# Optimization experiments

Measured on AMD Instinct MI355X. Metric: run time of the kernel, lower is better.

Reference implementation:

```python
import math
import jax, jax.numpy as jnp
import numpy as np

D_HEAD = 64
KS = 7
EPS = 1e-6


def _rope_freqs(d_head, n_heads):
    # AxialRoPE buffer: exp(linspace(log(pi), log(10*pi), nh*dim//4+1)[:-1]).view(dim//4, nh).T
    dim = d_head // 2
    n = n_heads * dim // 4
    f = np.exp(np.linspace(math.log(math.pi), math.log(10.0 * math.pi), n + 1)[:-1]).astype(np.float32)
    return jnp.asarray(f.reshape(dim // 4, n_heads).T)  # [nh, dim//4]


def setup_inputs() -> dict:
    key = jax.random.key(0)
    ks = jax.random.split(key, 6)
    B, C, T, H, W = 1, 512, 4, 32, 32
    cond_features = 256
    nh = C // D_HEAD
    x = jax.random.normal(ks[0], (B, C, T, H, W), dtype=jnp.float32)
    pos = jax.random.uniform(ks[1], (B, H, W, 2), dtype=jnp.float32)
    cond = jax.random.normal(ks[2], (B, cond_features), dtype=jnp.float32)
    # zero-init layers in the original (norm.linear, out_proj) get small random weights
    # here so the reference exercises nontrivial math/gradients.
    norm_w = jax.random.normal(ks[3], (cond_features, C), dtype=jnp.float32) * 0.02
    qkv_w = jax.random.normal(ks[4], (C, 3 * C), dtype=jnp.float32) * (1.0 / math.sqrt(C))
    out_w = jax.random.normal(ks[5], (C, C), dtype=jnp.float32) * (1.0 / math.sqrt(C))
    scale = jnp.full((nh,), 10.0, dtype=jnp.float32)
    return {"x": x, "pos": pos, "cond": cond, "norm_w": norm_w, "qkv_w": qkv_w,
            "scale": scale, "out_w": out_w}


def reference(x, pos, cond, norm_w, qkv_w, scale, out_w):
    B, C, T, H, W = x.shape
    nh = C // D_HEAD
    N = B * T
    skip = x

    # b c t h w -> (b t) h w c
    xr = jnp.transpose(x, (0, 2, 3, 4, 1)).reshape(N, H, W, C)
    condr = jnp.repeat(cond, T, axis=0)  # (b t) c, b-major

    # AdaRMSNorm: scale = linear(cond) + 1, applied with rms normalization
    s = condr @ norm_w + 1.0  # [N, C]
    mean_sq = jnp.mean(xr * xr, axis=-1, keepdims=True)
    xn = xr * (s[:, None, None, :] * jax.lax.rsqrt(mean_sq + EPS))

    qkv = (xn @ qkv_w).reshape(N, H, W, 3, nh, D_HEAD)
    q, k, v = qkv[:, :, :, 0], qkv[:, :, :, 1], qkv[:, :, :, 2]  # [N,H,W,nh,e]

    # cosine-sim scaling per head
    sqrt_scale = jnp.sqrt(scale)[:, None]  # [nh,1]
    q = q * (sqrt_scale * jax.lax.rsqrt(jnp.sum(q * q, -1, keepdims=True) + EPS))
    k = k * (sqrt_scale * jax.lax.rsqrt(jnp.sum(k * k, -1, keepdims=True) + EPS))

    # axial RoPE
    freqs = _rope_freqs(D_HEAD, nh)  # [nh, e//8]
    theta = jnp.concatenate([pos[..., None, 0:1] * freqs,
                             pos[..., None, 1:2] * freqs], axis=-1)  # [B,H,W,nh,e//4]
    theta = jnp.repeat(theta, T, axis=0)  # [N,H,W,nh,d]
    d = theta.shape[-1]
    cos_t, sin_t = jnp.cos(theta), jnp.sin(theta)

    def rope(t):
        x1, x2, x3 = t[..., :d], t[..., d:2 * d], t[..., 2 * d:]
        return jnp.concatenate([x1 * cos_t - x2 * sin_t,
                                x2 * cos_t + x1 * sin_t, x3], axis=-1)

    q, k = rope(q), rope(k)

    # neighborhood attention (NATTEN na2d semantics: window clamped to image border)
    r = KS // 2
    ih = jnp.clip(jnp.arange(H) - r, 0, H - KS)[:, None] + jnp.arange(KS)  # [H,KS]
    iw = jnp.clip(jnp.arange(W) - r, 0, W - KS)[:, None] + jnp.arange(KS)  # [W,KS]

    def windows(t):  # [N,H,W,nh,e] -> [N,H,W,KS*KS,nh,e]
        g = t[:, ih[:, :, None, None], iw[None, None, :, :]]  # [N,H,KS,W,KS,nh,e]
        return jnp.transpose(g, (0, 1, 3, 2, 4, 5, 6)).reshape(N, H, W, KS * KS, nh, D_HEAD)

    kw, vw = windows(k), windows(v)
    logits = jnp.einsum('nhwce,nhwkce->nhwck', q, kw)  # scale=1.0 in na2d call
    attn = jax.nn.softmax(logits, axis=-1)
    o = jnp.einsum('nhwck,nhwkce->nhwce', attn, vw).reshape(N, H, W, C)

    y = o @ out_w  # dropout=0.0
    y = jnp.transpose(y.reshape(B, T, H, W, C), (0, 4, 1, 2, 3))
    return y + skip
```

## Files before the change

### kernel.cpp

```cpp
#include <hip/hip_runtime.h>
#include <hip/hip_bf16.h>

typedef __hip_bfloat16 bf16;
#define F32(b) __bfloat162float(b)
#define B16(f) __float2bfloat16(f)

typedef __attribute__((ext_vector_type(8))) short short8;
typedef __attribute__((ext_vector_type(4))) float f32x4;

#define C_DIM 512
#define P_DIM 4096

__device__ __forceinline__ float wave_sum(float v){
#pragma unroll
  for (int o = 32; o > 0; o >>= 1) v += __shfl_xor(v, o, 64);
  return v;
}

__global__ __launch_bounds__(256) void k_prep_s(const float* __restrict__ cond,
                                                const float* __restrict__ norm_w,
                                                float* __restrict__ s){
  __shared__ float red[8][33];
  int c_l = threadIdx.x & 31, fo = threadIdx.x >> 5;
  int c = blockIdx.x * 32 + c_l;
  float acc = 0.f;
  for (int f = fo * 32; f < fo * 32 + 32; ++f)
    acc = fmaf(cond[f], norm_w[f * 512 + c], acc);
  red[fo][c_l] = acc;
  __syncthreads();
  if (threadIdx.x < 32){
    float a = 0.f;
#pragma unroll
    for (int i = 0; i < 8; ++i) a += red[i][c_l];
    s[blockIdx.x * 32 + c_l] = a + 1.0f;
  }
}

__global__ __launch_bounds__(256) void k_tables(const float* __restrict__ pos,
                                                float* __restrict__ cos_t,
                                                float* __restrict__ sin_t){
  int idx = blockIdx.x * 256 + threadIdx.x;
  int j  = idx & 15;
  int hd = (idx >> 4) & 7;
  int hw = idx >> 7;
  int axis = j >> 3;
  int i = j & 7;
  const float LOG_PI = 1.1447298858494002f;
  const float LOG10F = 2.302585092994046f;
  float f = expf(LOG_PI + (float)(i * 8 + hd) * (LOG10F / 64.0f));
  float th = pos[hw * 2 + axis] * f;
  cos_t[idx] = cosf(th);
  sin_t[idx] = sinf(th);
}

__global__ __launch_bounds__(256) void k_rms(const float* __restrict__ x,
                                             float* __restrict__ rms_ss){
  __shared__ float red[4][64];
  int bp = blockIdx.x & 63, bc = blockIdx.x >> 6;
  int co = threadIdx.x >> 6, pl = threadIdx.x & 63;
  int p = bp * 64 + pl;
  float acc = 0.f;
  for (int c = bc * 64 + co; c < bc * 64 + 64; c += 4){
    float v = x[c * P_DIM + p];
    acc = fmaf(v, v, acc);
  }
  red[co][pl] = acc;
  __syncthreads();
  if (threadIdx.x < 64){
    int q = threadIdx.x;
    float ss = red[0][q] + red[1][q] + red[2][q] + red[3][q];
    atomicAdd(&rms_ss[bp * 64 + q], ss);
  }
}

__global__ __launch_bounds__(256) void k_castwT(const float* __restrict__ qkv_w,
                                                const float* __restrict__ out_w,
                                                bf16* __restrict__ qkvT,
                                                bf16* __restrict__ outT){
  __shared__ float tile[64][65];
  int bid = blockIdx.x;
  const float* src; bf16* dst; int NW, n0, c0;
  if (bid < 192){ src = qkv_w; dst = qkvT; NW = 1536; n0 = (bid % 24) * 64; c0 = (bid / 24) * 64; }
  else { int b = bid - 192; src = out_w; dst = outT; NW = 512; n0 = (b & 7) * 64; c0 = (b >> 3) * 64; }
  int grp = threadIdx.x >> 6, lane = threadIdx.x & 63;
  for (int i = grp; i < 64; i += 4)
    tile[i][lane] = src[(c0 + i) * NW + n0 + lane];
  __syncthreads();
  for (int j = grp; j < 64; j += 4)
    dst[(n0 + j) * 512 + c0 + lane] = B16(tile[lane][j]);
}

__global__ __launch_bounds__(256) void k_xnt(const float* __restrict__ x,
                                             const float* __restrict__ s,
                                             const float* __restrict__ rms_ss,
                                             bf16* __restrict__ xn){
  __shared__ float tile[64][65];
  int bp = blockIdx.x & 63, bc = blockIdx.x >> 6;
  int p0 = bp * 64, c0 = bc * 64;
  int grp = threadIdx.x >> 6, lane = threadIdx.x & 63;
  for (int i = grp; i < 64; i += 4)
    tile[i][lane] = x[(c0 + i) * P_DIM + p0 + lane] * s[c0 + i];
  __syncthreads();
  for (int j = grp; j < 64; j += 4){
    float rv = rsqrtf(rms_ss[p0 + j] * (1.0f / 512.0f) + 1e-6f);
    xn[(size_t)(p0 + j) * 512 + c0 + lane] = B16(tile[lane][j] * rv);
  }
}

__global__ __launch_bounds__(256) void k_gemm_qkv(const bf16* __restrict__ Ab,
                                                  const bf16* __restrict__ BTb,
                                                  bf16* __restrict__ qkv_bf){
  __shared__ unsigned short a_t[64 * 40];
  __shared__ unsigned short b_t[64 * 40];
  const unsigned short* A  = (const unsigned short*)Ab;
  const unsigned short* BT = (const unsigned short*)BTb;
  int m0 = blockIdx.x * 64;
  int n0 = blockIdx.y * 64;
  int tid = threadIdx.x;
  int w = tid >> 6, l = tid & 63;
  int rsel = tid >> 2, seg = tid & 3;

  f32x4 acc[4];
#pragma unroll
  for (int j = 0; j < 4; ++j)
#pragma unroll
    for (int r = 0; r < 4; ++r) acc[j][r] = 0.f;

  int lrow = w * 16 + (l & 15);
  int quad = l >> 4;

  for (int kk = 0; kk < 512; kk += 32){
    *(uint4*)&a_t[rsel * 40 + seg * 8] = *(const uint4*)&A[(size_t)(m0 + rsel) * 512 + kk + seg * 8];
    *(uint4*)&b_t[rsel * 40 + seg * 8] = *(const uint4*)&BT[(size_t)(n0 + rsel) * 512 + kk + seg * 8];
    __syncthreads();
    short8 af = *(const short8*)&a_t[lrow * 40 + quad * 8];
#pragma unroll
    for (int j = 0; j < 4; ++j){
      short8 bfr = *(const short8*)&b_t[(j * 16 + (l & 15)) * 40 + quad * 8];
      acc[j] = __builtin_amdgcn_mfma_f32_16x16x32_bf16(af, bfr, acc[j], 0, 0, 0);
    }
    __syncthreads();
  }
  int cb = l & 15;
#pragma unroll
  for (int j = 0; j < 4; ++j){
    int col = n0 + j * 16 + cb;
#pragma unroll
    for (int r = 0; r < 4; ++r){
      int rowg = m0 + w * 16 + (l >> 4) * 4 + r;
      qkv_bf[(size_t)rowg * 1536 + col] = B16(acc[j][r]);
    }
  }
}

__global__ __launch_bounds__(256) void k_normrope(bf16* __restrict__ qkv_bf,
                                                  const float* __restrict__ scale,
                                                  const float* __restrict__ cos_t,
                                                  const float* __restrict__ sin_t){
  int u = blockIdx.x * 4 + (threadIdx.x >> 6);
  int d = threadIdx.x & 63;
  int p = u >> 4;
  int r = u & 15;
  int head = r >> 1;
  int qk = r & 1;
  size_t base = (size_t)p * 1536 + qk * 512 + head * 64;
  float v = F32(qkv_bf[base + d]);
  float ss = wave_sum(v * v);
  v *= sqrtf(scale[head]) * rsqrtf(ss + 1e-6f);
  float partner = __shfl_xor(v, 16, 64);
  int cb = ((p & 1023) * 8 + head) * 16;
  float outv;
  if (d < 16)       outv = v * cos_t[cb + d]      - partner * sin_t[cb + d];
  else if (d < 32)  outv = v * cos_t[cb + d - 16] + partner * sin_t[cb + d - 16];
  else              outv = v;
  qkv_bf[base + d] = B16(outv);
}

#define KL_S 80
#define VT_S 232
#define PP_S 232
__global__ __launch_bounds__(256) void k_attn(const bf16* __restrict__ qkv_bfp,
                                              bf16* __restrict__ o_bf){
  __shared__ unsigned short kp[208 * KL_S];
  __shared__ unsigned short vT[64 * VT_S];
  const unsigned short* qkv = (const unsigned short*)qkv_bfp;

  int bid = blockIdx.x;
  int head = bid & 7;
  int patch = bid >> 3;
  int t = patch >> 4;
  int ph = (patch >> 2) & 3, pw = patch & 3;
  int h0 = ph * 8, w0 = pw * 8;
  int rs = min(max(h0 - 3, 0), 18);
  int cs = min(max(w0 - 3, 0), 18);
  int tbase = t << 10;
  int tid = threadIdx.x;
  int cp = tid & 31, pxg = tid >> 5;

  for (int i = 0; i < 26; ++i){
    int px = i * 8 + pxg;
    unsigned val = 0;
    if (px < 196){
      int rr = px / 14, cc = px - rr * 14;
      size_t pn = (size_t)(tbase + (rs + rr) * 32 + (cs + cc));
      val = *(const unsigned*)&qkv[pn * 1536 + 512 + head * 64 + cp * 2];
    }
    *(unsigned*)&kp[px * KL_S + cp * 2] = val;
  }
  for (int i = 0; i < 14; ++i){
    int pp = i * 8 + pxg;
    int px0 = 2 * pp, px1 = px0 + 1;
    unsigned v0 = 0, v1 = 0;
    if (px0 < 196){
      int rr = px0 / 14, cc = px0 - rr * 14;
      size_t pn = (size_t)(tbase + (rs + rr) * 32 + (cs + cc));
      v0 = *(const unsigned*)&qkv[pn * 1536 + 1024 + head * 64 + cp * 2];
    }
    if (px1 < 196){
      int rr = px1 / 14, cc = px1 - rr * 14;
      size_t pn = (size_t)(tbase + (rs + rr) * 32 + (cs + cc));
      v1 = *(const unsigned*)&qkv[pn * 1536 + 1024 + head * 64 + cp * 2];
    }
    unsigned lo = (v0 & 0xffffu) | (v1 << 16);
    unsigned hi = (v0 >> 16) | (v1 & 0xffff0000u);
    *(unsigned*)&vT[(2 * cp) * VT_S + 2 * pp] = lo;
    *(unsigned*)&vT[(2 * cp + 1) * VT_S + 2 * pp] = hi;
  }

  int w = tid >> 6, l = tid & 63;
  int g = l >> 4, cb = l & 15;

  int q_a = w * 16 + cb;
  size_t abase = (size_t)(tbase + (h0 + (q_a >> 3)) * 32 + (w0 + (q_a & 7))) * 1536 + head * 64;
  short8 qa0 = *(const short8*)&qkv[abase + g * 8];
  short8 qa1 = *(const short8*)&qkv[abase + 32 + g * 8];

  __syncthreads();

  f32x4 acc[13];
#pragma unroll
  for (int nt = 0; nt < 13; ++nt)
#pragma unroll
    for (int r = 0; r < 4; ++r) acc[nt][r] = 0.f;
#pragma unroll
  for (int nt = 0; nt < 13; ++nt){
    short8 kb0 = *(const short8*)&kp[(nt * 16 + cb) * KL_S + g * 8];
    short8 kb1 = *(const short8*)&kp[(nt * 16 + cb) * KL_S + 32 + g * 8];
    acc[nt] = __builtin_amdgcn_mfma_f32_16x16x32_bf16(qa0, kb0, acc[nt], 0, 0, 0);
    acc[nt] = __builtin_amdgcn_mfma_f32_16x16x32_bf16(qa1, kb1, acc[nt], 0, 0, 0);
  }
  __syncthreads();

  int wr0[4], wc0[4];
#pragma unroll
  for (int r = 0; r < 4; ++r){
    int q_l = w * 16 + g * 4 + r;
    int hq = h0 + (q_l >> 3), wq = w0 + (q_l & 7);
    wr0[r] = min(max(hq - 3, 0), 25) - rs;
    wc0[r] = min(max(wq - 3, 0), 25) - cs;
  }
  float mx[4] = {-1e30f, -1e30f, -1e30f, -1e30f};
#pragma unroll
  for (int nt = 0; nt < 13; ++nt){
    int kg = nt * 16 + cb;
    int kr = kg / 14, kc = kg - kr * 14;
    bool kvalid = kg < 196;
#pragma unroll
    for (int r = 0; r < 4; ++r){
      bool v = kvalid && ((unsigned)(kr - wr0[r]) < 7u) && ((unsigned)(kc - wc0[r]) < 7u);
      float lg = v ? acc[nt][r] : -1e30f;
      acc[nt][r] = lg;
      mx[r] = fmaxf(mx[r], lg);
    }
  }
#pragma unroll
  for (int off = 1; off < 16; off <<= 1)
#pragma unroll
    for (int r = 0; r < 4; ++r) mx[r] = fmaxf(mx[r], __shfl_xor(mx[r], off, 64));
  float sm[4] = {0.f, 0.f, 0.f, 0.f};
#pragma unroll
  for (int nt = 0; nt < 13; ++nt)
#pragma unroll
    for (int r = 0; r < 4; ++r){
      float e = __expf(acc[nt][r] - mx[r]);
      acc[nt][r] = e;
      sm[r] += e;
    }
#pragma unroll
  for (int off = 1; off < 16; off <<= 1)
#pragma unroll
    for (int r = 0; r < 4; ++r) sm[r] += __shfl_xor(sm[r], off, 64);
  float inv[4];
#pragma unroll
  for (int r = 0; r < 4; ++r) inv[r] = 1.0f / sm[r];

#pragma unroll
  for (int nt = 0; nt < 13; ++nt)
#pragma unroll
    for (int r = 0; r < 4; ++r)
      *reinterpret_cast<bf16*>(&kp[(w * 16 + g * 4 + r) * PP_S + nt * 16 + cb]) = B16(acc[nt][r] * inv[r]);
#pragma unroll
  for (int r = 0; r < 4; ++r)
    kp[(w * 16 + g * 4 + r) * PP_S + 208 + cb] = 0;
  __syncthreads();

  f32x4 acc2[4];
#pragma unroll
  for (int ct = 0; ct < 4; ++ct)
#pragma unroll
    for (int r = 0; r < 4; ++r) acc2[ct][r] = 0.f;
#pragma unroll
  for (int kt = 0; kt < 7; ++kt){
    short8 pa = *(const short8*)&kp[(w * 16 + cb) * PP_S + kt * 32 + g * 8];
#pragma unroll
    for (int ct = 0; ct < 4; ++ct){
      short8 vb = *(const short8*)&vT[(ct * 16 + cb) * VT_S + kt * 32 + g * 8];
      acc2[ct] = __builtin_amdgcn_mfma_f32_16x16x32_bf16(pa, vb, acc2[ct], 0, 0, 0);
    }
  }
#pragma unroll
  for (int ct = 0; ct < 4; ++ct)
#pragma unroll
    for (int r = 0; r < 4; ++r){
      int q_l = w * 16 + g * 4 + r;
      int p = tbase + (h0 + (q_l >> 3)) * 32 + (w0 + (q_l & 7));
      o_bf[(size_t)p * 512 + head * 64 + ct * 16 + cb] = B16(acc2[ct][r]);
    }
}

__global__ __launch_bounds__(256) void k_gemm_out(const bf16* __restrict__ Ab,
                                                  const bf16* __restrict__ BTb,
                                                  const float* __restrict__ xres,
                                                  float* __restrict__ out){
  __shared__ unsigned short a_t[64 * 40];
  __shared__ unsigned short b_t[64 * 40];
  __shared__ float tile[64][65];
  const unsigned short* A  = (const unsigned short*)Ab;
  const unsigned short* BT = (const unsigned short*)BTb;
  int m0 = blockIdx.x * 64;
  int n0 = blockIdx.y * 64;
  int tid = threadIdx.x;
  int w = tid >> 6, l = tid & 63;
  int rsel = tid >> 2, seg = tid & 3;

  f32x4 acc[4];
#pragma unroll
  for (int j = 0; j < 4; ++j)
#pragma unroll
    for (int r = 0; r < 4; ++r) acc[j][r] = 0.f;

  int lrow = w * 16 + (l & 15);
  int quad = l >> 4;

  for (int kk = 0; kk < 512; kk += 32){
    *(uint4*)&a_t[rsel * 40 + seg * 8] = *(const uint4*)&A[(size_t)(m0 + rsel) * 512 + kk + seg * 8];
    *(uint4*)&b_t[rsel * 40 + seg * 8] = *(const uint4*)&BT[(size_t)(n0 + rsel) * 512 + kk + seg * 8];
    __syncthreads();
    short8 af = *(const short8*)&a_t[lrow * 40 + quad * 8];
#pragma unroll
    for (int j = 0; j < 4; ++j){
      short8 bfr = *(const short8*)&b_t[(j * 16 + (l & 15)) * 40 + quad * 8];
      acc[j] = __builtin_amdgcn_mfma_f32_16x16x32_bf16(af, bfr, acc[j], 0, 0, 0);
    }
    __syncthreads();
  }
  int cb = l & 15;
#pragma unroll
  for (int j = 0; j < 4; ++j)
#pragma unroll
    for (int r = 0; r < 4; ++r)
      tile[w * 16 + (l >> 4) * 4 + r][j * 16 + cb] = acc[j][r];
  __syncthreads();
  int grp = tid >> 6, lane = tid & 63;
  for (int j2 = grp; j2 < 64; j2 += 4){
    int c = n0 + j2;
    int p = m0 + lane;
    out[(size_t)c * P_DIM + p] = tile[lane][j2] + xres[(size_t)c * P_DIM + p];
  }
}

extern "C" void kernel_launch(void* const* d_in, const int* in_sizes, int n_in,
                              void* d_out, int out_size, void* d_ws, size_t ws_size,
                              hipStream_t stream){
  const float* x      = (const float*)d_in[0];
  const float* pos    = (const float*)d_in[1];
  const float* cond   = (const float*)d_in[2];
  const float* norm_w = (const float*)d_in[3];
  const float* qkv_w  = (const float*)d_in[4];
  const float* scale  = (const float*)d_in[5];
  const float* out_w  = (const float*)d_in[6];
  float* out = (float*)d_out;

  char* wp = (char*)d_ws;
  auto alloc = [&](size_t bytes) -> char* {
    char* r = wp;
    wp += (bytes + 255) & ~((size_t)255);
    return r;
  };
  float* s_f    = (float*)alloc(512 * 4);
  float* rms_ss = (float*)alloc(4096 * 4);
  float* cos_t  = (float*)alloc(131072 * 4);
  float* sin_t  = (float*)alloc(131072 * 4);
  bf16*  xn     = (bf16*) alloc((size_t)4096 * 512 * 2);
  bf16*  qkvT   = (bf16*) alloc((size_t)1536 * 512 * 2);
  bf16*  outT   = (bf16*) alloc((size_t)512 * 512 * 2);
  bf16*  qkv_bf = (bf16*) alloc((size_t)4096 * 1536 * 2);
  bf16*  o_bf   = (bf16*) alloc((size_t)4096 * 512 * 2);

  hipMemsetAsync(rms_ss, 0, 4096 * 4, stream);
  k_prep_s  <<<16,          256, 0, stream>>>(cond, norm_w, s_f);
  k_tables  <<<512,         256, 0, stream>>>(pos, cos_t, sin_t);
  k_rms     <<<512,         256, 0, stream>>>(x, rms_ss);
  k_castwT  <<<256,         256, 0, stream>>>(qkv_w, out_w, qkvT, outT);
  k_xnt     <<<512,         256, 0, stream>>>(x, s_f, rms_ss, xn);
  k_gemm_qkv<<<dim3(64,24), 256, 0, stream>>>(xn, qkvT, qkv_bf);
  k_normrope<<<16384,       256, 0, stream>>>(qkv_bf, scale, cos_t, sin_t);
  k_attn    <<<512,         256, 0, stream>>>(qkv_bf, o_bf);
  k_gemm_out<<<dim3(64,8),  256, 0, stream>>>(o_bf, outT, x, out);
}
```

Before: 158.7 us.

## Enlarge GEMM tiles, compute RoPE inline, replace atomics with partial sums

Both GEMMs now use 128x64 block tiles with a K step of 64. Each wave computes a 2x4 grid of MFMA tiles, which gives more reuse of A and B fragments and halves the number of barriers. The separate cos/sin table kernel is removed, and RoPE angles are computed inline in k_normrope with fast intrinsics. The RMS reduction writes per-channel-block partial sums, which k_xnt adds up, so the memset and atomics are no longer needed. The trade-offs are fewer blocks (768 and 256) on a large GPU, possible accuracy loss from __cosf/__sinf, and more partial-sum reads in k_xnt.

```diff
diff --git a/kernel.cpp b/kernel.cpp
--- a/kernel.cpp
+++ b/kernel.cpp
@@ -36,25 +36,8 @@
   }
 }
 
-__global__ __launch_bounds__(256) void k_tables(const float* __restrict__ pos,
-                                                float* __restrict__ cos_t,
-                                                float* __restrict__ sin_t){
-  int idx = blockIdx.x * 256 + threadIdx.x;
-  int j  = idx & 15;
-  int hd = (idx >> 4) & 7;
-  int hw = idx >> 7;
-  int axis = j >> 3;
-  int i = j & 7;
-  const float LOG_PI = 1.1447298858494002f;
-  const float LOG10F = 2.302585092994046f;
-  float f = expf(LOG_PI + (float)(i * 8 + hd) * (LOG10F / 64.0f));
-  float th = pos[hw * 2 + axis] * f;
-  cos_t[idx] = cosf(th);
-  sin_t[idx] = sinf(th);
-}
-
 __global__ __launch_bounds__(256) void k_rms(const float* __restrict__ x,
-                                             float* __restrict__ rms_ss){
+                                             float* __restrict__ rms_part){
   __shared__ float red[4][64];
   int bp = blockIdx.x & 63, bc = blockIdx.x >> 6;
   int co = threadIdx.x >> 6, pl = threadIdx.x & 63;
@@ -68,8 +51,7 @@
   __syncthreads();
   if (threadIdx.x < 64){
     int q = threadIdx.x;
-    float ss = red[0][q] + red[1][q] + red[2][q] + red[3][q];
-    atomicAdd(&rms_ss[bp * 64 + q], ss);
+    rms_part[bc * P_DIM + bp * 64 + q] = red[0][q] + red[1][q] + red[2][q] + red[3][q];
   }
 }
 
@@ -92,7 +74,7 @@
 
 __global__ __launch_bounds__(256) void k_xnt(const float* __restrict__ x,
                                              const float* __restrict__ s,
-                                             const float* __restrict__ rms_ss,
+                                             const float* __restrict__ rms_part,
                                              bf16* __restrict__ xn){
   __shared__ float tile[64][65];
   int bp = blockIdx.x & 63, bc = blockIdx.x >> 6;
@@ -102,61 +84,81 @@
     tile[i][lane] = x[(c0 + i) * P_DIM + p0 + lane] * s[c0 + i];
   __syncthreads();
   for (int j = grp; j < 64; j += 4){
-    float rv = rsqrtf(rms_ss[p0 + j] * (1.0f / 512.0f) + 1e-6f);
+    float ss = 0.f;
+#pragma unroll
+    for (int i = 0; i < 8; ++i) ss += rms_part[i * P_DIM + p0 + j];
+    float rv = rsqrtf(ss * (1.0f / 512.0f) + 1e-6f);
     xn[(size_t)(p0 + j) * 512 + c0 + lane] = B16(tile[lane][j] * rv);
   }
 }
 
+#define AS 72
 __global__ __launch_bounds__(256) void k_gemm_qkv(const bf16* __restrict__ Ab,
                                                   const bf16* __restrict__ BTb,
                                                   bf16* __restrict__ qkv_bf){
-  __shared__ unsigned short a_t[64 * 40];
-  __shared__ unsigned short b_t[64 * 40];
+  __shared__ unsigned short a_t[128 * AS];
+  __shared__ unsigned short b_t[64 * AS];
   const unsigned short* A  = (const unsigned short*)Ab;
   const unsigned short* BT = (const unsigned short*)BTb;
-  int m0 = blockIdx.x * 64;
+  int m0 = blockIdx.x * 128;
   int n0 = blockIdx.y * 64;
   int tid = threadIdx.x;
-  int w = tid >> 6, l = tid & 63;
-  int rsel = tid >> 2, seg = tid & 3;
-
-  f32x4 acc[4];
-#pragma unroll
-  for (int j = 0; j < 4; ++j)
-#pragma unroll
-    for (int r = 0; r < 4; ++r) acc[j][r] = 0.f;
-
-  int lrow = w * 16 + (l & 15);
-  int quad = l >> 4;
-
-  for (int kk = 0; kk < 512; kk += 32){
-    *(uint4*)&a_t[rsel * 40 + seg * 8] = *(const uint4*)&A[(size_t)(m0 + rsel) * 512 + kk + seg * 8];
-    *(uint4*)&b_t[rsel * 40 + seg * 8] = *(const uint4*)&BT[(size_t)(n0 + rsel) * 512 + kk + seg * 8];
-    __syncthreads();
-    short8 af = *(const short8*)&a_t[lrow * 40 + quad * 8];
-#pragma unroll
-    for (int j = 0; j < 4; ++j){
-      short8 bfr = *(const short8*)&b_t[(j * 16 + (l & 15)) * 40 + quad * 8];
-      acc[j] = __builtin_amdgcn_mfma_f32_16x16x32_bf16(af, bfr, acc[j], 0, 0, 0);
-    }
-    __syncthreads();
-  }
-  int cb = l & 15;
-#pragma unroll
-  for (int j = 0; j < 4; ++j){
-    int col = n0 + j * 16 + cb;
-#pragma unroll
-    for (int r = 0; r < 4; ++r){
-      int rowg = m0 + w * 16 + (l >> 4) * 4 + r;
-      qkv_bf[(size_t)rowg * 1536 + col] = B16(acc[j][r]);
-    }
-  }
+  int w = tid >> 6, l = tid & 63, g = l >> 4, cb = l & 15;
+
+  f32x4 acc[2][4];
+#pragma unroll
+  for (int mi = 0; mi < 2; ++mi)
+#pragma unroll
+    for (int nj = 0; nj < 4; ++nj)
+#pragma unroll
+      for (int r = 0; r < 4; ++r) acc[mi][nj][r] = 0.f;
+
+  for (int kk = 0; kk < 512; kk += 64){
+#pragma unroll
+    for (int i = 0; i < 4; ++i){
+      int sid = tid + i * 256;
+      int row = sid >> 3, seg = sid & 7;
+      *(uint4*)&a_t[row * AS + seg * 8] = *(const uint4*)&A[(size_t)(m0 + row) * 512 + kk + seg * 8];
+    }
+#pragma unroll
+    for (int i = 0; i < 2; ++i){
+      int sid = tid + i * 256;
+      int row = sid >> 3, seg = sid & 7;
+      *(uint4*)&b_t[row * AS + seg * 8] = *(const uint4*)&BT[(size_t)(n0 + row) * 512 + kk + seg * 8];
+    }
+    __syncthreads();
+#pragma unroll
+    for (int kc = 0; kc < 2; ++kc){
+      short8 af[2];
+#pragma unroll
+      for (int mi = 0; mi < 2; ++mi)
+        af[mi] = *(const short8*)&a_t[(w * 32 + mi * 16 + cb) * AS + kc * 32 + g * 8];
+#pragma unroll
+      for (int nj = 0; nj < 4; ++nj){
+        short8 bfr = *(const short8*)&b_t[(nj * 16 + cb) * AS + kc * 32 + g * 8];
+#pragma unroll
+        for (int mi = 0; mi < 2; ++mi)
+          acc[mi][nj] = __builtin_amdgcn_mfma_f32_16x16x32_bf16(af[mi], bfr, acc[mi][nj], 0, 0, 0);
+      }
+    }
+    __syncthreads();
+  }
+#pragma unroll
+  for (int mi = 0; mi < 2; ++mi)
+#pragma unroll
+    for (int nj = 0; nj < 4; ++nj){
+      int col = n0 + nj * 16 + cb;
+#pragma unroll
+      for (int r = 0; r < 4; ++r){
+        int rowg = m0 + w * 32 + mi * 16 + g * 4 + r;
+        qkv_bf[(size_t)rowg * 1536 + col] = B16(acc[mi][nj][r]);
+      }
+    }
 }
 
 __global__ __launch_bounds__(256) void k_normrope(bf16* __restrict__ qkv_bf,
                                                   const float* __restrict__ scale,
-                                                  const float* __restrict__ cos_t,
-                                                  const float* __restrict__ sin_t){
+                                                  const float* __restrict__ pos){
   int u = blockIdx.x * 4 + (threadIdx.x >> 6);
   int d = threadIdx.x & 63;
   int p = u >> 4;
@@ -168,10 +170,16 @@
   float ss = wave_sum(v * v);
   v *= sqrtf(scale[head]) * rsqrtf(ss + 1e-6f);
   float partner = __shfl_xor(v, 16, 64);
-  int cb = ((p & 1023) * 8 + head) * 16;
+  int j = d & 15;
+  int axis = j >> 3, i = j & 7;
+  const float LOG_PI = 1.1447298858494002f;
+  const float LOG10F = 2.302585092994046f;
+  float f = __expf(LOG_PI + (float)(i * 8 + head) * (LOG10F / 64.0f));
+  float th = pos[(p & 1023) * 2 + axis] * f;
+  float ct = __cosf(th), st = __sinf(th);
   float outv;
-  if (d < 16)       outv = v * cos_t[cb + d]      - partner * sin_t[cb + d];
-  else if (d < 32)  outv = v * cos_t[cb + d - 16] + partner * sin_t[cb + d - 16];
+  if (d < 16)       outv = v * ct - partner * st;
+  else if (d < 32)  outv = v * ct + partner * st;
   else              outv = v;
   qkv_bf[base + d] = B16(outv);
 }
@@ -332,50 +340,73 @@
                                                   const bf16* __restrict__ BTb,
                                                   const float* __restrict__ xres,
                                                   float* __restrict__ out){
-  __shared__ unsigned short a_t[64 * 40];
-  __shared__ unsigned short b_t[64 * 40];
+  __shared__ unsigned short a_t[128 * AS];
+  __shared__ unsigned short b_t[64 * AS];
   __shared__ float tile[64][65];
   const unsigned short* A  = (const unsigned short*)Ab;
   const unsigned short* BT = (const unsigned short*)BTb;
-  int m0 = blockIdx.x * 64;
+  int m0 = blockIdx.x * 128;
   int n0 = blockIdx.y * 64;
   int tid = threadIdx.x;
-  int w = tid >> 6, l = tid & 63;
-  int rsel = tid >> 2, seg = tid & 3;
-
-  f32x4 acc[4];
-#pragma unroll
-  for (int j = 0; j < 4; ++j)
-#pragma unroll
-    for (int r = 0; r < 4; ++r) acc[j][r] = 0.f;
-
-  int lrow = w * 16 + (l & 15);
-  int quad = l >> 4;
-
-  for (int kk = 0; kk < 512; kk += 32){
-    *(uint4*)&a_t[rsel * 40 + seg * 8] = *(const uint4*)&A[(size_t)(m0 + rsel) * 512 + kk + seg * 8];
-    *(uint4*)&b_t[rsel * 40 + seg * 8] = *(const uint4*)&BT[(size_t)(n0 + rsel) * 512 + kk + seg * 8];
-    __syncthreads();
-    short8 af = *(const short8*)&a_t[lrow * 40 + quad * 8];
-#pragma unroll
-    for (int j = 0; j < 4; ++j){
-      short8 bfr = *(const short8*)&b_t[(j * 16 + (l & 15)) * 40 + quad * 8];
-      acc[j] = __builtin_amdgcn_mfma_f32_16x16x32_bf16(af, bfr, acc[j], 0, 0, 0);
-    }
-    __syncthreads();
-  }
-  int cb = l & 15;
-#pragma unroll
-  for (int j = 0; j < 4; ++j)
-#pragma unroll
-    for (int r = 0; r < 4; ++r)
-      tile[w * 16 + (l >> 4) * 4 + r][j * 16 + cb] = acc[j][r];
-  __syncthreads();
+  int w = tid >> 6, l = tid & 63, g = l >> 4, cb = l & 15;
+
+  f32x4 acc[2][4];
+#pragma unroll
+  for (int mi = 0; mi < 2; ++mi)
+#pragma unroll
+    for (int nj = 0; nj < 4; ++nj)
+#pragma unroll
+      for (int r = 0; r < 4; ++r) acc[mi][nj][r] = 0.f;
+
+  for (int kk = 0; kk < 512; kk += 64){
+#pragma unroll
+    for (int i = 0; i < 4; ++i){
+      int sid = tid + i * 256;
+      int row = sid >> 3, seg = sid & 7;
+      *(uint4*)&a_t[row * AS + seg * 8] = *(const uint4*)&A[(size_t)(m0 + row) * 512 + kk + seg * 8];
+    }
+#pragma unroll
+    for (int i = 0; i < 2; ++i){
+      int sid = tid + i * 256;
+      int row = sid >> 3, seg = sid & 7;
+      *(uint4*)&b_t[row * AS + seg * 8] = *(const uint4*)&BT[(size_t)(n0 + row) * 512 + kk + seg * 8];
+    }
+    __syncthreads();
+#pragma unroll
+    for (int kc = 0; kc < 2; ++kc){
+      short8 af[2];
+#pragma unroll
+      for (int mi = 0; mi < 2; ++mi)
+        af[mi] = *(const short8*)&a_t[(w * 32 + mi * 16 + cb) * AS + kc * 32 + g * 8];
+#pragma unroll
+      for (int nj = 0; nj < 4; ++nj){
+        short8 bfr = *(const short8*)&b_t[(nj * 16 + cb) * AS + kc * 32 + g * 8];
+#pragma unroll
+        for (int mi = 0; mi < 2; ++mi)
+          acc[mi][nj] = __builtin_amdgcn_mfma_f32_16x16x32_bf16(af[mi], bfr, acc[mi][nj], 0, 0, 0);
+      }
+    }
+    __syncthreads();
+  }
   int grp = tid >> 6, lane = tid & 63;
-  for (int j2 = grp; j2 < 64; j2 += 4){
-    int c = n0 + j2;
-    int p = m0 + lane;
-    out[(size_t)c * P_DIM + p] = tile[lane][j2] + xres[(size_t)c * P_DIM + p];
+#pragma unroll
+  for (int hh = 0; hh < 2; ++hh){
+    __syncthreads();
+    if ((w >> 1) == hh){
+#pragma unroll
+      for (int mi = 0; mi < 2; ++mi)
+#pragma unroll
+        for (int nj = 0; nj < 4; ++nj)
+#pragma unroll
+          for (int r = 0; r < 4; ++r)
+            tile[(w & 1) * 32 + mi * 16 + g * 4 + r][nj * 16 + cb] = acc[mi][nj][r];
+    }
+    __syncthreads();
+    for (int j2 = grp; j2 < 64; j2 += 4){
+      int c = n0 + j2;
+      int p = m0 + hh * 64 + lane;
+      out[(size_t)c * P_DIM + p] = tile[lane][j2] + xres[(size_t)c * P_DIM + p];
+    }
   }
 }
 
@@ -397,24 +428,20 @@
     wp += (bytes + 255) & ~((size_t)255);
     return r;
   };
-  float* s_f    = (float*)alloc(512 * 4);
-  float* rms_ss = (float*)alloc(4096 * 4);
-  float* cos_t  = (float*)alloc(131072 * 4);
-  float* sin_t  = (float*)alloc(131072 * 4);
-  bf16*  xn     = (bf16*) alloc((size_t)4096 * 512 * 2);
-  bf16*  qkvT   = (bf16*) alloc((size_t)1536 * 512 * 2);
-  bf16*  outT   = (bf16*) alloc((size_t)512 * 512 * 2);
-  bf16*  qkv_bf = (bf16*) alloc((size_t)4096 * 1536 * 2);
-  bf16*  o_bf   = (bf16*) alloc((size_t)4096 * 512 * 2);
-
-  hipMemsetAsync(rms_ss, 0, 4096 * 4, stream);
+  float* s_f      = (float*)alloc(512 * 4);
+  float* rms_part = (float*)alloc(8 * 4096 * 4);
+  bf16*  xn       = (bf16*) alloc((size_t)4096 * 512 * 2);
+  bf16*  qkvT     = (bf16*) alloc((size_t)1536 * 512 * 2);
+  bf16*  outT     = (bf16*) alloc((size_t)512 * 512 * 2);
+  bf16*  qkv_bf   = (bf16*) alloc((size_t)4096 * 1536 * 2);
+  bf16*  o_bf     = (bf16*) alloc((size_t)4096 * 512 * 2);
+
   k_prep_s  <<<16,          256, 0, stream>>>(cond, norm_w, s_f);
-  k_tables  <<<512,         256, 0, stream>>>(pos, cos_t, sin_t);
-  k_rms     <<<512,         256, 0, stream>>>(x, rms_ss);
+  k_rms     <<<512,         256, 0, stream>>>(x, rms_part);
   k_castwT  <<<256,         256, 0, stream>>>(qkv_w, out_w, qkvT, outT);
-  k_xnt     <<<512,         256, 0, stream>>>(x, s_f, rms_ss, xn);
-  k_gemm_qkv<<<dim3(64,24), 256, 0, stream>>>(xn, qkvT, qkv_bf);
-  k_normrope<<<16384,       256, 0, stream>>>(qkv_bf, scale, cos_t, sin_t);
+  k_xnt     <<<512,         256, 0, stream>>>(x, s_f, rms_part, xn);
+  k_gemm_qkv<<<dim3(32,24), 256, 0, stream>>>(xn, qkvT, qkv_bf);
+  k_normrope<<<16384,       256, 0, stream>>>(qkv_bf, scale, pos);
   k_attn    <<<512,         256, 0, stream>>>(qkv_bf, o_bf);
-  k_gemm_out<<<dim3(64,8),  256, 0, stream>>>(o_bf, outT, x, out);
-}
+  k_gemm_out<<<dim3(32,8),  256, 0, stream>>>(o_bf, outT, x, out);
+}
```

After: 155.1 us. 2.2% less time.
